# Kernel tuning notes

Measured on AMD Instinct MI355X. Metric: run time of the kernel, lower is better.

## Reference

```python
import jax, jax.numpy as jnp
import numpy as np

N_NODES = 18870
HIDDEN = 256
K = 20
HEAD_HIDDEN = 512
N_CLASSES = 3
N_GENES_OUT = 6640
B = 1024
FALLBACK_SCALE = 1e-3
LN_EPS = 1e-5


def setup_inputs() -> dict:
    key = jax.random.key(0)
    ks = jax.random.split(key, 8)
    node_idx = jax.random.randint(ks[0], (B,), 0, N_NODES)
    topk_neighbors = jax.random.randint(ks[1], (N_NODES, K), 0, N_NODES)
    node_emb = jax.random.normal(ks[2], (N_NODES, HIDDEN), dtype=jnp.float32)
    fallback_emb = jax.random.normal(ks[3], (HIDDEN,), dtype=jnp.float32) * 0.02
    w_attn = jax.random.normal(ks[4], (HIDDEN,), dtype=jnp.float32) * 0.02
    ln_gamma = jnp.ones((2 * HIDDEN,), dtype=jnp.float32)
    ln_beta = jnp.zeros((2 * HIDDEN,), dtype=jnp.float32)
    W1 = jax.random.normal(ks[5], (2 * HIDDEN, HEAD_HIDDEN), dtype=jnp.float32) * 0.02
    b1 = jnp.zeros((HEAD_HIDDEN,), dtype=jnp.float32)
    W2 = jax.random.normal(ks[6], (HEAD_HIDDEN, N_CLASSES * N_GENES_OUT), dtype=jnp.float32) * 0.02
    b2 = jnp.zeros((N_CLASSES * N_GENES_OUT,), dtype=jnp.float32)
    return dict(node_idx=node_idx, topk_neighbors=topk_neighbors, node_emb=node_emb,
                fallback_emb=fallback_emb, w_attn=w_attn, ln_gamma=ln_gamma, ln_beta=ln_beta,
                W1=W1, b1=b1, W2=W2, b2=b2)


def reference(node_idx, topk_neighbors, node_emb, fallback_emb, w_attn,
              ln_gamma, ln_beta, W1, b1, W2, b2):
    valid = node_idx >= 0                                   # [B]
    safe_idx = jnp.where(valid, node_idx, 0)                # [B]
    graph_emb = node_emb[safe_idx]                          # [B, H]
    pert_emb = jnp.where(valid[:, None],
                         graph_emb + FALLBACK_SCALE * fallback_emb[None, :],
                         fallback_emb[None, :])              # [B, H]

    nbr_idx = topk_neighbors[safe_idx]                      # [B, K]
    valid_nbr = nbr_idx >= 0                                # [B, K]
    nbr_emb = node_emb[jnp.clip(nbr_idx, 0)]                # [B, K, H]
    nbr_emb = nbr_emb * valid_nbr[..., None].astype(nbr_emb.dtype)

    # Faithful to the original broadcast: scores[b,k] = pert_emb[b,0] * (nbr_emb[b,k] . w_attn)
    scores = pert_emb[:, 0:1] * jnp.einsum('bkh,h->bk', nbr_emb, w_attn)  # [B, K]
    scores = jnp.where(valid_nbr, scores, -1e9)
    has_valid = jnp.any(valid_nbr, axis=1, keepdims=True)   # [B, 1]
    attn = jnp.where(has_valid, jax.nn.softmax(scores, axis=-1),
                     jnp.zeros_like(scores))                # [B, K]
    context = jnp.einsum('bk,bkh->bh', attn, nbr_emb)       # [B, H]

    combined = jnp.concatenate([pert_emb, context], axis=-1)  # [B, 2H]
    mu = jnp.mean(combined, axis=-1, keepdims=True)
    var = jnp.mean(jnp.square(combined - mu), axis=-1, keepdims=True)
    x = (combined - mu) * jax.lax.rsqrt(var + LN_EPS) * ln_gamma + ln_beta
    h = jax.nn.gelu(x @ W1 + b1, approximate=False)          # [B, HH]
    logits = h @ W2 + b2                                     # [B, 3*6640]
    return logits.reshape(-1, N_CLASSES, N_GENES_OUT)


if __name__ == '__main__':
    out = reference(**setup_inputs())
    print(out.shape)
```

## Files before the change

kernel.cpp:

```cpp
#include <hip/hip_runtime.h>
#include <hip/hip_bf16.h>
#include <math.h>

#define HIDDEN 256
#define K_NBR 20
#define NB 1024

typedef __bf16 bf16x8 __attribute__((ext_vector_type(8)));
typedef float f32x4 __attribute__((ext_vector_type(4)));

__device__ __forceinline__ float wave_sum(float v) {
#pragma unroll
    for (int o = 32; o > 0; o >>= 1) v += __shfl_xor(v, o, 64);
    return v;
}

__device__ __forceinline__ void gload16(const void* g, void* l) {
    __builtin_amdgcn_global_load_lds(
        (const __attribute__((address_space(1))) void*)g,
        (__attribute__((address_space(3))) void*)l, 16, 0, 0);
}

__device__ __forceinline__ int swz_chunk(int g, int row) {
    return (g & ~7) | ((g & 7) ^ (row & 7));
}

__device__ __forceinline__ void attn_ln_body(
    int b, int t, const int* __restrict__ node_idx, const int* __restrict__ topk,
    const float* __restrict__ node_emb, const float* __restrict__ fallback,
    const float* __restrict__ w_attn, const float* __restrict__ gamma,
    const float* __restrict__ beta, __bf16* __restrict__ xb, int swz_on,
    float* pe, float (*nbr)[HIDDEN], int* nidx, float* sc, float* red)
{
    int lane = t & 63, w = t >> 6;

    int nid = node_idx[b];
    bool valid = nid >= 0;
    int safe = valid ? nid : 0;

    pe[t] = valid ? node_emb[(size_t)safe * HIDDEN + t] + 1e-3f * fallback[t]
                  : fallback[t];
    if (t < K_NBR) nidx[t] = topk[safe * K_NBR + t];
    __syncthreads();

    for (int r = 0; r < K_NBR; ++r) {
        int gi = nidx[r];
        nbr[r][t] = (gi >= 0) ? node_emb[(size_t)gi * HIDDEN + t] : 0.f;
    }
    __syncthreads();

    float pe0 = pe[0];
    float wa[4];
#pragma unroll
    for (int q = 0; q < 4; ++q) wa[q] = w_attn[lane + 64 * q];
    for (int k = w; k < K_NBR; k += 4) {
        float p = 0.f;
#pragma unroll
        for (int q = 0; q < 4; ++q) p += nbr[k][lane + 64 * q] * wa[q];
        p = wave_sum(p);
        if (lane == 0) sc[k] = (nidx[k] >= 0) ? pe0 * p : -1e9f;
    }
    __syncthreads();

    bool has_valid = false;
#pragma unroll
    for (int k = 0; k < K_NBR; ++k) has_valid |= (nidx[k] >= 0);
    float mx = -1e30f;
#pragma unroll
    for (int k = 0; k < K_NBR; ++k) mx = fmaxf(mx, sc[k]);
    float at[K_NBR];
    float s = 0.f;
#pragma unroll
    for (int k = 0; k < K_NBR; ++k) { at[k] = expf(sc[k] - mx); s += at[k]; }
    float inv = has_valid ? 1.f / s : 0.f;

    float ctx = 0.f;
#pragma unroll
    for (int k = 0; k < K_NBR; ++k) ctx += (at[k] * inv) * nbr[k][t];

    float v0 = pe[t], v1 = ctx;
    float s1 = wave_sum(v0 + v1);
    float s2 = wave_sum(v0 * v0 + v1 * v1);
    if (lane == 0) { red[w] = s1; red[4 + w] = s2; }
    __syncthreads();
    s1 = red[0] + red[1] + red[2] + red[3];
    s2 = red[4] + red[5] + red[6] + red[7];
    float mu = s1 / 512.f;
    float var = s2 / 512.f - mu * mu;
    float rs = rsqrtf(var + 1e-5f);

    size_t base = (size_t)b * 512;
    int mask = swz_on ? (b & 7) : 0;
    {
        int e = t;
        int g = e >> 3, off = e & 7;
        int gp = (g & ~7) | ((g & 7) ^ mask);
        xb[base + gp * 8 + off] = (__bf16)((v0 - mu) * rs * gamma[t] + beta[t]);
        e = 256 + t;
        g = e >> 3;
        gp = (g & ~7) | ((g & 7) ^ mask);
        xb[base + gp * 8 + off] = (__bf16)((v1 - mu) * rs * gamma[256 + t] + beta[256 + t]);
    }
}

__device__ __forceinline__ void transpose_body(
    const float* __restrict__ Wm, __bf16* __restrict__ WT,
    int Kd, int Nd, int Np, int bx, int by, int t)
{
    int n = bx * 64 + (t >> 2);
    int k0 = by * 32 + (t & 3) * 8;
    bool ok = n < Nd;
    bf16x8 v;
#pragma unroll
    for (int j = 0; j < 8; ++j) {
        float f = ok ? Wm[(size_t)(k0 + j) * Nd + n] : 0.f;
        v[j] = (__bf16)f;
    }
    if (n < Np) {
        int gp = swz_chunk(k0 >> 3, n);
        *(bf16x8*)(WT + (size_t)n * Kd + gp * 8) = v;
    }
}

__global__ __launch_bounds__(256) void prep_kernel(
    const int* __restrict__ node_idx, const int* __restrict__ topk,
    const float* __restrict__ node_emb, const float* __restrict__ fallback,
    const float* __restrict__ w_attn, const float* __restrict__ gamma,
    const float* __restrict__ beta, const float* __restrict__ W1,
    const float* __restrict__ W2, __bf16* __restrict__ xb,
    __bf16* __restrict__ w1t, __bf16* __restrict__ w2t)
{
    __shared__ float pe[HIDDEN];
    __shared__ float nbr[K_NBR][HIDDEN];
    __shared__ int   nidx[K_NBR];
    __shared__ float sc[K_NBR];
    __shared__ float red[8];

    int bid = blockIdx.x;
    int t = threadIdx.x;
    if (bid < 4992) {
        transpose_body(W2, w2t, 512, 19920, 19968, bid % 312, bid / 312, t);
        return;
    }
    bid -= 4992;
    if (bid < 128) {
        transpose_body(W1, w1t, 512, 512, 512, bid % 8, bid / 8, t);
        return;
    }
    bid -= 128;
    attn_ln_body(bid, t, node_idx, topk, node_emb, fallback, w_attn, gamma, beta,
                 xb, 1, pe, nbr, nidx, sc, red);
}

__global__ __launch_bounds__(256) void attn_ln_kernel(
    const int* __restrict__ node_idx, const int* __restrict__ topk,
    const float* __restrict__ node_emb, const float* __restrict__ fallback,
    const float* __restrict__ w_attn, const float* __restrict__ gamma,
    const float* __restrict__ beta, __bf16* __restrict__ xb, int swz_on)
{
    __shared__ float pe[HIDDEN];
    __shared__ float nbr[K_NBR][HIDDEN];
    __shared__ int   nidx[K_NBR];
    __shared__ float sc[K_NBR];
    __shared__ float red[8];
    attn_ln_body(blockIdx.x, threadIdx.x, node_idx, topk, node_emb, fallback,
                 w_attn, gamma, beta, xb, swz_on, pe, nbr, nidx, sc, red);
}

__global__ __launch_bounds__(256, 4) void gemm1_kernel(
    const __bf16* __restrict__ A, const __bf16* __restrict__ BT,
    const float* __restrict__ bias, __bf16* __restrict__ Cb,
    int M, int N, int K)
{
    constexpr int BK = 64;
    __shared__ __bf16 As[2][64 * BK];
    __shared__ __bf16 Bs[2][64 * BK];

    int t = threadIdx.x;
    int lane = t & 63;
    int wid = t >> 6;
    int wm = wid >> 1, wn = wid & 1;
    int lo = lane & 15, hi = lane >> 4;

    int nwg = gridDim.x;
    int bid = blockIdx.x;
    int cpx = nwg >> 3;
    int lid = (bid & 7) * cpx + (bid >> 3);
    int m0 = (lid & 15) * 64;
    int n0 = (lid >> 4) * 64;

    int rsub = lane >> 3, kc = lane & 7;

    auto STAGE = [&](int buf, int k0) {
#pragma unroll
        for (int j = 0; j < 2; ++j) {
            int rb = j * 32 + wid * 8;
            gload16(A + (size_t)(m0 + rb + rsub) * K + k0 + kc * 8, &As[buf][rb * BK]);
        }
#pragma unroll
        for (int j = 0; j < 2; ++j) {
            int rb = j * 32 + wid * 8;
            gload16(BT + (size_t)(n0 + rb + rsub) * K + k0 + kc * 8, &Bs[buf][rb * BK]);
        }
    };

    f32x4 acc[2][2];
#pragma unroll
    for (int m = 0; m < 2; ++m)
#pragma unroll
        for (int n = 0; n < 2; ++n)
            acc[m][n] = (f32x4){0.f, 0.f, 0.f, 0.f};

    auto COMPUTE = [&](int buf) {
#pragma unroll
        for (int ks = 0; ks < 2; ++ks) {
            bf16x8 af[2], bfr[2];
#pragma unroll
            for (int m = 0; m < 2; ++m) {
                int r = wm * 32 + m * 16 + lo;
                af[m] = *(const bf16x8*)&As[buf][r * BK + (((ks * 4 + hi) ^ (r & 7)) * 8)];
            }
#pragma unroll
            for (int n = 0; n < 2; ++n) {
                int r = wn * 32 + n * 16 + lo;
                bfr[n] = *(const bf16x8*)&Bs[buf][r * BK + (((ks * 4 + hi) ^ (r & 7)) * 8)];
            }
#pragma unroll
            for (int m = 0; m < 2; ++m)
#pragma unroll
                for (int n = 0; n < 2; ++n)
                    acc[m][n] = __builtin_amdgcn_mfma_f32_16x16x32_bf16(
                        af[m], bfr[n], acc[m][n], 0, 0, 0);
        }
    };

    const int nt = K / BK;
    STAGE(0, 0);
    for (int tt = 0; tt < nt - 1; ++tt) {
        STAGE((tt + 1) & 1, (tt + 1) * BK);
        asm volatile("s_waitcnt vmcnt(4)" ::: "memory");
        __builtin_amdgcn_s_barrier();
        __builtin_amdgcn_sched_barrier(0);
        COMPUTE(tt & 1);
        __builtin_amdgcn_sched_barrier(0);
        __builtin_amdgcn_s_barrier();
    }
    asm volatile("s_waitcnt vmcnt(0)" ::: "memory");
    __builtin_amdgcn_s_barrier();
    __builtin_amdgcn_sched_barrier(0);
    COMPUTE((nt - 1) & 1);

#pragma unroll
    for (int m = 0; m < 2; ++m) {
        int gr = m0 + wm * 32 + m * 16 + hi * 4;
#pragma unroll
        for (int n = 0; n < 2; ++n) {
            int gc = n0 + wn * 32 + n * 16 + lo;
            float bv = bias[gc];
#pragma unroll
            for (int r = 0; r < 4; ++r) {
                float v = acc[m][n][r] + bv;
                float g = v * 0.5f * (1.f + erff(v * 0.70710678118f));
                int row = gr + r;
                int gp = swz_chunk(gc >> 3, row);
                Cb[(size_t)row * N + gp * 8 + (gc & 7)] = (__bf16)g;
            }
        }
    }
}

__global__ __launch_bounds__(512, 4) void gemm2_kernel(
    const __bf16* __restrict__ A, const __bf16* __restrict__ BT,
    const float* __restrict__ bias, float* __restrict__ C,
    int M, int N, int K)
{
    constexpr int BK = 64;
    __shared__ __bf16 As[2][128 * BK];
    __shared__ __bf16 Bs[2][128 * BK];

    int t = threadIdx.x;
    int lane = t & 63;
    int wid = t >> 6;
    int wm = wid >> 2, wn = wid & 3;
    int lo = lane & 15, hi = lane >> 4;

    int nwg = gridDim.x;
    int bid = blockIdx.x;
    int cpx = nwg >> 3;
    int lid = (bid & 7) * cpx + (bid >> 3);
    int m0 = (lid & 7) * 128;
    int n0 = (lid >> 3) * 128;

    int rsub = lane >> 3, kc = lane & 7;

    auto STAGE = [&](int buf, int k0) {
#pragma unroll
        for (int j = 0; j < 2; ++j) {
            int rb = j * 64 + wid * 8;
            gload16(A + (size_t)(m0 + rb + rsub) * K + k0 + kc * 8, &As[buf][rb * BK]);
        }
#pragma unroll
        for (int j = 0; j < 2; ++j) {
            int rb = j * 64 + wid * 8;
            gload16(BT + (size_t)(n0 + rb + rsub) * K + k0 + kc * 8, &Bs[buf][rb * BK]);
        }
    };

    f32x4 acc[4][2];
#pragma unroll
    for (int m = 0; m < 4; ++m)
#pragma unroll
        for (int n = 0; n < 2; ++n)
            acc[m][n] = (f32x4){0.f, 0.f, 0.f, 0.f};

    auto COMPUTE = [&](int buf) {
#pragma unroll
        for (int ks = 0; ks < 2; ++ks) {
            bf16x8 af[4], bfr[2];
#pragma unroll
            for (int m = 0; m < 4; ++m) {
                int r = wm * 64 + m * 16 + lo;
                af[m] = *(const bf16x8*)&As[buf][r * BK + (((ks * 4 + hi) ^ (r & 7)) * 8)];
            }
#pragma unroll
            for (int n = 0; n < 2; ++n) {
                int r = wn * 32 + n * 16 + lo;
                bfr[n] = *(const bf16x8*)&Bs[buf][r * BK + (((ks * 4 + hi) ^ (r & 7)) * 8)];
            }
#pragma unroll
            for (int m = 0; m < 4; ++m)
#pragma unroll
                for (int n = 0; n < 2; ++n)
                    acc[m][n] = __builtin_amdgcn_mfma_f32_16x16x32_bf16(
                        af[m], bfr[n], acc[m][n], 0, 0, 0);
        }
    };

    const int nt = K / BK;
    STAGE(0, 0);
    for (int tt = 0; tt < nt - 1; ++tt) {
        STAGE((tt + 1) & 1, (tt + 1) * BK);
        asm volatile("s_waitcnt vmcnt(4)" ::: "memory");
        __builtin_amdgcn_s_barrier();
        __builtin_amdgcn_sched_barrier(0);
        COMPUTE(tt & 1);
        __builtin_amdgcn_sched_barrier(0);
        __builtin_amdgcn_s_barrier();
    }
    asm volatile("s_waitcnt vmcnt(0)" ::: "memory");
    __builtin_amdgcn_s_barrier();
    __builtin_amdgcn_sched_barrier(0);
    COMPUTE((nt - 1) & 1);

#pragma unroll
    for (int m = 0; m < 4; ++m) {
        int gr = m0 + wm * 64 + m * 16 + hi * 4;
#pragma unroll
        for (int n = 0; n < 2; ++n) {
            int gc = n0 + wn * 32 + n * 16 + lo;
            if (gc < N) {
                float bv = bias[gc];
#pragma unroll
                for (int r = 0; r < 4; ++r)
                    C[(size_t)(gr + r) * N + gc] = acc[m][n][r] + bv;
            }
        }
    }
}

template<bool GELU>
__global__ __launch_bounds__(256) void gemm_kernel(
    const __bf16* __restrict__ A, const float* __restrict__ Bm,
    const float* __restrict__ bias, float* __restrict__ Cf, __bf16* __restrict__ Cb,
    int M, int N, int K)
{
    constexpr int BK = 64;
    __shared__ bf16x8 As[2][128 * 8];
    __shared__ bf16x8 Bs[2][128 * 8];

    int t = threadIdx.x;
    int lane = t & 63;
    int wid = t >> 6;
    int wm = wid >> 1, wn = wid & 1;
    int lo = lane & 15, hi = lane >> 4;

    int n0 = blockIdx.x * 128;
    int m0 = blockIdx.y * 128;

    int cA = t & 7;
    int rA = t >> 3;
    int nl = t & 127;
    int kcb = t >> 7;

    bf16x8 a_st[4];
    bf16x8 b_st[4];

    auto LOAD = [&](int k0) {
#pragma unroll
        for (int i = 0; i < 4; ++i)
            a_st[i] = *(const bf16x8*)(A + (size_t)(m0 + rA + 32 * i) * K + k0 + cA * 8);
        int col = n0 + nl;
        bool ok = col < N;
#pragma unroll
        for (int i = 0; i < 4; ++i) {
            int kcv = kcb + 2 * i;
            bf16x8 v;
#pragma unroll
            for (int j = 0; j < 8; ++j) {
                float f = ok ? Bm[(size_t)(k0 + kcv * 8 + j) * N + col] : 0.f;
                v[j] = (__bf16)f;
            }
            b_st[i] = v;
        }
    };
    auto WRITE = [&](int buf) {
#pragma unroll
        for (int i = 0; i < 4; ++i) {
            int r = rA + 32 * i;
            As[buf][r * 8 + (cA ^ (r & 7))] = a_st[i];
        }
#pragma unroll
        for (int i = 0; i < 4; ++i) {
            int kcv = kcb + 2 * i;
            Bs[buf][nl * 8 + (kcv ^ (nl & 7))] = b_st[i];
        }
    };

    f32x4 acc[4][4];
#pragma unroll
    for (int m = 0; m < 4; ++m)
#pragma unroll
        for (int n = 0; n < 4; ++n)
            acc[m][n] = (f32x4){0.f, 0.f, 0.f, 0.f};

    auto COMPUTE = [&](int buf) {
#pragma unroll
        for (int ks = 0; ks < 2; ++ks) {
            bf16x8 af[4], bfr[4];
#pragma unroll
            for (int m = 0; m < 4; ++m) {
                int r = wm * 64 + m * 16 + lo;
                af[m] = As[buf][r * 8 + ((ks * 4 + hi) ^ (r & 7))];
            }
#pragma unroll
            for (int n = 0; n < 4; ++n) {
                int r = wn * 64 + n * 16 + lo;
                bfr[n] = Bs[buf][r * 8 + ((ks * 4 + hi) ^ (r & 7))];
            }
#pragma unroll
            for (int m = 0; m < 4; ++m)
#pragma unroll
                for (int n = 0; n < 4; ++n)
                    acc[m][n] = __builtin_amdgcn_mfma_f32_16x16x32_bf16(
                        af[m], bfr[n], acc[m][n], 0, 0, 0);
        }
    };

    const int nt = K / BK;
    LOAD(0);
    WRITE(0);
    __syncthreads();
    for (int tt = 0; tt < nt; ++tt) {
        int cur = tt & 1;
        if (tt + 1 < nt) LOAD((tt + 1) * BK);
        COMPUTE(cur);
        if (tt + 1 < nt) WRITE(cur ^ 1);
        __syncthreads();
    }

#pragma unroll
    for (int m = 0; m < 4; ++m) {
        int gr = m0 + wm * 64 + m * 16 + hi * 4;
#pragma unroll
        for (int n = 0; n < 4; ++n) {
            int gc = n0 + wn * 64 + n * 16 + lo;
            if (gc < N) {
                float bv = bias[gc];
#pragma unroll
                for (int r = 0; r < 4; ++r) {
                    float v = acc[m][n][r] + bv;
                    if constexpr (GELU) {
                        float g = v * 0.5f * (1.f + erff(v * 0.70710678118f));
                        Cb[(size_t)(gr + r) * N + gc] = (__bf16)g;
                    } else {
                        Cf[(size_t)(gr + r) * N + gc] = v;
                    }
                }
            }
        }
    }
}

extern "C" void kernel_launch(void* const* d_in, const int* in_sizes, int n_in,
                              void* d_out, int out_size, void* d_ws, size_t ws_size,
                              hipStream_t stream) {
    const int*   node_idx = (const int*)d_in[0];
    const int*   topk     = (const int*)d_in[1];
    const float* node_emb = (const float*)d_in[2];
    const float* fallback = (const float*)d_in[3];
    const float* w_attn   = (const float*)d_in[4];
    const float* gamma    = (const float*)d_in[5];
    const float* beta     = (const float*)d_in[6];
    const float* W1       = (const float*)d_in[7];
    const float* b1       = (const float*)d_in[8];
    const float* W2       = (const float*)d_in[9];
    const float* b2       = (const float*)d_in[10];
    float* out = (float*)d_out;

    const int M = 1024, Kd = 512, N1 = 512, N2 = 19920;
    const int N2p = 19968;

    __bf16* xb  = (__bf16*)d_ws;
    __bf16* h   = xb + (size_t)M * Kd;
    __bf16* w1t = h + (size_t)M * Kd;
    __bf16* w2t = w1t + (size_t)N1 * Kd;
    size_t needed = ((size_t)2 * M * Kd + (size_t)N1 * Kd + (size_t)N2p * Kd) * sizeof(__bf16);

    if (ws_size >= needed) {
        prep_kernel<<<4992 + 128 + 1024, 256, 0, stream>>>(
            node_idx, topk, node_emb, fallback, w_attn, gamma, beta, W1, W2,
            xb, w1t, w2t);

        gemm1_kernel<<<dim3(128), 256, 0, stream>>>(
            xb, w1t, b1, h, M, N1, Kd);

        gemm2_kernel<<<dim3(1248), 512, 0, stream>>>(
            h, w2t, b2, out, M, N2, Kd);
    } else {
        attn_ln_kernel<<<NB, 256, 0, stream>>>(node_idx, topk, node_emb, fallback,
                                               w_attn, gamma, beta, xb, 0);
        gemm_kernel<true><<<dim3(4, 8), 256, 0, stream>>>(
            xb, W1, b1, nullptr, h, M, N1, Kd);
        gemm_kernel<false><<<dim3(156, 8), 256, 0, stream>>>(
            h, W2, b2, out, nullptr, M, N2, Kd);
    }
}
```

Measured before the change: 74.73 us.

## Fuse prep, GEMM1 and GEMM2 into one persistent cooperative kernel with grid syncs

Replaces the three launches (prep/transpose, gemm1, gemm2) with one persistent cooperative kernel of 512-thread blocks. It loops over work units and separates the stages with grid-wide syncs. Attention is processed two rows per block, the W2 transpose uses nontemporal loads, and GEMM1 tiles widen to 64x128. The goal is to remove launch overhead and the tail bubbles between kernels, at the cost of grid-sync latency and limited occupancy from the 64 KB shared memory. It falls back to the old three-kernel path if the cooperative launch fails.

```diff
diff --git a/kernel.cpp b/kernel.cpp
--- a/kernel.cpp
+++ b/kernel.cpp
@@ -1,6 +1,9 @@
 #include <hip/hip_runtime.h>
 #include <hip/hip_bf16.h>
+#include <hip/hip_cooperative_groups.h>
 #include <math.h>
+
+namespace cg = cooperative_groups;
 
 #define HIDDEN 256
 #define K_NBR 20
@@ -21,8 +24,335 @@
         (__attribute__((address_space(3))) void*)l, 16, 0, 0);
 }
 
-__device__ __forceinline__ int swz_chunk(int g, int row) {
+__device__ __forceinline__ int swz3(int g, int row) {
     return (g & ~7) | ((g & 7) ^ (row & 7));
+}
+
+struct AttnSmem {
+    float pe[2][HIDDEN];
+    float nbr[2][K_NBR][HIDDEN];
+    int   nidx[2][K_NBR];
+    float sc[2][K_NBR];
+    float red[2][8];
+};
+
+__device__ void attn2_unit(int p, int t,
+    const int* node_idx, const int* topk, const float* node_emb,
+    const float* fallback, const float* w_attn, const float* gamma,
+    const float* beta, __bf16* xb, void* smem)
+{
+    AttnSmem& S = *(AttnSmem*)smem;
+    int s = t >> 8, tl = t & 255;
+    int lane = tl & 63, w = tl >> 6;
+    int b = p * 2 + s;
+
+    int nid = node_idx[b];
+    bool valid = nid >= 0;
+    int safe = valid ? nid : 0;
+
+    S.pe[s][tl] = valid ? node_emb[(size_t)safe * HIDDEN + tl] + 1e-3f * fallback[tl]
+                        : fallback[tl];
+    if (tl < K_NBR) S.nidx[s][tl] = topk[safe * K_NBR + tl];
+    __syncthreads();
+
+    for (int r = 0; r < K_NBR; ++r) {
+        int gi = S.nidx[s][r];
+        S.nbr[s][r][tl] = (gi >= 0) ? node_emb[(size_t)gi * HIDDEN + tl] : 0.f;
+    }
+    __syncthreads();
+
+    float pe0 = S.pe[s][0];
+    float wa[4];
+#pragma unroll
+    for (int q = 0; q < 4; ++q) wa[q] = w_attn[lane + 64 * q];
+    for (int k = w; k < K_NBR; k += 4) {
+        float pp = 0.f;
+#pragma unroll
+        for (int q = 0; q < 4; ++q) pp += S.nbr[s][k][lane + 64 * q] * wa[q];
+        pp = wave_sum(pp);
+        if (lane == 0) S.sc[s][k] = (S.nidx[s][k] >= 0) ? pe0 * pp : -1e9f;
+    }
+    __syncthreads();
+
+    bool has_valid = false;
+#pragma unroll
+    for (int k = 0; k < K_NBR; ++k) has_valid |= (S.nidx[s][k] >= 0);
+    float mx = -1e30f;
+#pragma unroll
+    for (int k = 0; k < K_NBR; ++k) mx = fmaxf(mx, S.sc[s][k]);
+    float at[K_NBR];
+    float sm = 0.f;
+#pragma unroll
+    for (int k = 0; k < K_NBR; ++k) { at[k] = expf(S.sc[s][k] - mx); sm += at[k]; }
+    float inv = has_valid ? 1.f / sm : 0.f;
+
+    float ctx = 0.f;
+#pragma unroll
+    for (int k = 0; k < K_NBR; ++k) ctx += (at[k] * inv) * S.nbr[s][k][tl];
+
+    float v0 = S.pe[s][tl], v1 = ctx;
+    float s1 = wave_sum(v0 + v1);
+    float s2 = wave_sum(v0 * v0 + v1 * v1);
+    if (lane == 0) { S.red[s][w] = s1; S.red[s][4 + w] = s2; }
+    __syncthreads();
+    s1 = S.red[s][0] + S.red[s][1] + S.red[s][2] + S.red[s][3];
+    s2 = S.red[s][4] + S.red[s][5] + S.red[s][6] + S.red[s][7];
+    float mu = s1 / 512.f;
+    float var = s2 / 512.f - mu * mu;
+    float rs = rsqrtf(var + 1e-5f);
+
+    size_t base = (size_t)b * 512;
+    int mask = b & 7;
+    {
+        int e = tl;
+        int g = e >> 3, off = e & 7;
+        int gp = (g & ~7) | ((g & 7) ^ mask);
+        xb[base + gp * 8 + off] = (__bf16)((v0 - mu) * rs * gamma[tl] + beta[tl]);
+        e = 256 + tl;
+        g = e >> 3;
+        gp = (g & ~7) | ((g & 7) ^ mask);
+        xb[base + gp * 8 + off] = (__bf16)((v1 - mu) * rs * gamma[256 + tl] + beta[256 + tl]);
+    }
+    __syncthreads();
+}
+
+__device__ void transpose_unit(const float* __restrict__ Wm, __bf16* __restrict__ WT,
+                               int Kd, int Nd, int Np, int ux, int uy, int t)
+{
+    int n = ux * 128 + (t >> 2);
+    int k0 = uy * 32 + (t & 3) * 8;
+    bool ok = n < Nd;
+    bf16x8 v;
+#pragma unroll
+    for (int j = 0; j < 8; ++j) {
+        float f = ok ? __builtin_nontemporal_load(&Wm[(size_t)(k0 + j) * Nd + n]) : 0.f;
+        v[j] = (__bf16)f;
+    }
+    if (n < Np) {
+        int gp = swz3(k0 >> 3, n);
+        *(bf16x8*)(WT + (size_t)n * Kd + gp * 8) = v;
+    }
+}
+
+__device__ void gemm1_tile(int bid, int t, void* smem,
+    const __bf16* __restrict__ A, const __bf16* __restrict__ BT,
+    const float* __restrict__ bias, __bf16* __restrict__ Cb)
+{
+    const int K = 512, N = 512;
+    __bf16* As = (__bf16*)smem;
+    __bf16* Bs = (__bf16*)smem + 8192;
+
+    int lane = t & 63, wid = t >> 6;
+    int wm = wid >> 2, wn = wid & 3;
+    int lo = lane & 15, hi = lane >> 4;
+    int m0 = (bid & 15) * 64;
+    int n0 = (bid >> 4) * 128;
+    int rsub = lane >> 3, kc = lane & 7;
+
+    auto STAGE = [&](int buf, int k0) {
+        gload16(A + (size_t)(m0 + wid * 8 + rsub) * K + k0 + kc * 8,
+                &As[buf * 4096 + wid * 512]);
+#pragma unroll
+        for (int j = 0; j < 2; ++j) {
+            int rb = j * 64 + wid * 8;
+            gload16(BT + (size_t)(n0 + rb + rsub) * K + k0 + kc * 8,
+                    &Bs[buf * 8192 + rb * 64]);
+        }
+    };
+
+    f32x4 acc[2][2];
+#pragma unroll
+    for (int m = 0; m < 2; ++m)
+#pragma unroll
+        for (int n = 0; n < 2; ++n)
+            acc[m][n] = (f32x4){0.f, 0.f, 0.f, 0.f};
+
+    auto COMPUTE = [&](int buf) {
+#pragma unroll
+        for (int ks = 0; ks < 2; ++ks) {
+            bf16x8 af[2], bfr[2];
+#pragma unroll
+            for (int m = 0; m < 2; ++m) {
+                int r = wm * 32 + m * 16 + lo;
+                af[m] = *(const bf16x8*)&As[buf * 4096 + r * 64 + (((ks * 4 + hi) ^ (r & 7)) * 8)];
+            }
+#pragma unroll
+            for (int n = 0; n < 2; ++n) {
+                int r = wn * 32 + n * 16 + lo;
+                bfr[n] = *(const bf16x8*)&Bs[buf * 8192 + r * 64 + (((ks * 4 + hi) ^ (r & 7)) * 8)];
+            }
+#pragma unroll
+            for (int m = 0; m < 2; ++m)
+#pragma unroll
+                for (int n = 0; n < 2; ++n)
+                    acc[m][n] = __builtin_amdgcn_mfma_f32_16x16x32_bf16(
+                        af[m], bfr[n], acc[m][n], 0, 0, 0);
+        }
+    };
+
+    const int nt = K / 64;
+    STAGE(0, 0);
+    for (int tt = 0; tt < nt - 1; ++tt) {
+        STAGE((tt + 1) & 1, (tt + 1) * 64);
+        asm volatile("s_waitcnt vmcnt(3)" ::: "memory");
+        __builtin_amdgcn_s_barrier();
+        __builtin_amdgcn_sched_barrier(0);
+        COMPUTE(tt & 1);
+        __builtin_amdgcn_sched_barrier(0);
+        __builtin_amdgcn_s_barrier();
+    }
+    asm volatile("s_waitcnt vmcnt(0)" ::: "memory");
+    __builtin_amdgcn_s_barrier();
+    __builtin_amdgcn_sched_barrier(0);
+    COMPUTE((nt - 1) & 1);
+    __builtin_amdgcn_s_barrier();
+
+#pragma unroll
+    for (int m = 0; m < 2; ++m) {
+        int gr = m0 + wm * 32 + m * 16 + hi * 4;
+#pragma unroll
+        for (int n = 0; n < 2; ++n) {
+            int gc = n0 + wn * 32 + n * 16 + lo;
+            float bv = bias[gc];
+#pragma unroll
+            for (int r = 0; r < 4; ++r) {
+                float v = acc[m][n][r] + bv;
+                float g = v * 0.5f * (1.f + erff(v * 0.70710678118f));
+                int row = gr + r;
+                int gp = swz3(gc >> 3, row);
+                Cb[(size_t)row * N + gp * 8 + (gc & 7)] = (__bf16)g;
+            }
+        }
+    }
+}
+
+__device__ void gemm2_tile(int tile, int t, void* smem,
+    const __bf16* __restrict__ A, const __bf16* __restrict__ BT,
+    const float* __restrict__ bias, float* __restrict__ C, int N)
+{
+    const int K = 512;
+    __bf16* As = (__bf16*)smem;
+    __bf16* Bs = (__bf16*)smem + 16384;
+
+    int lane = t & 63, wid = t >> 6;
+    int wm = wid >> 2, wn = wid & 3;
+    int lo = lane & 15, hi = lane >> 4;
+
+    int lid = (tile & 7) * 156 + (tile >> 3);
+    int m0 = (lid & 7) * 128;
+    int n0 = (lid >> 3) * 128;
+
+    int rsub = lane >> 3, kc = lane & 7;
+
+    auto STAGE = [&](int buf, int k0) {
+#pragma unroll
+        for (int j = 0; j < 2; ++j) {
+            int rb = j * 64 + wid * 8;
+            gload16(A + (size_t)(m0 + rb + rsub) * K + k0 + kc * 8, &As[buf * 8192 + rb * 64]);
+        }
+#pragma unroll
+        for (int j = 0; j < 2; ++j) {
+            int rb = j * 64 + wid * 8;
+            gload16(BT + (size_t)(n0 + rb + rsub) * K + k0 + kc * 8, &Bs[buf * 8192 + rb * 64]);
+        }
+    };
+
+    f32x4 acc[4][2];
+#pragma unroll
+    for (int m = 0; m < 4; ++m)
+#pragma unroll
+        for (int n = 0; n < 2; ++n)
+            acc[m][n] = (f32x4){0.f, 0.f, 0.f, 0.f};
+
+    auto COMPUTE = [&](int buf) {
+#pragma unroll
+        for (int ks = 0; ks < 2; ++ks) {
+            bf16x8 af[4], bfr[2];
+#pragma unroll
+            for (int m = 0; m < 4; ++m) {
+                int r = wm * 64 + m * 16 + lo;
+                af[m] = *(const bf16x8*)&As[buf * 8192 + r * 64 + (((ks * 4 + hi) ^ (r & 7)) * 8)];
+            }
+#pragma unroll
+            for (int n = 0; n < 2; ++n) {
+                int r = wn * 32 + n * 16 + lo;
+                bfr[n] = *(const bf16x8*)&Bs[buf * 8192 + r * 64 + (((ks * 4 + hi) ^ (r & 7)) * 8)];
+            }
+#pragma unroll
+            for (int m = 0; m < 4; ++m)
+#pragma unroll
+                for (int n = 0; n < 2; ++n)
+                    acc[m][n] = __builtin_amdgcn_mfma_f32_16x16x32_bf16(
+                        af[m], bfr[n], acc[m][n], 0, 0, 0);
+        }
+    };
+
+    const int nt = K / 64;
+    STAGE(0, 0);
+    for (int tt = 0; tt < nt - 1; ++tt) {
+        STAGE((tt + 1) & 1, (tt + 1) * 64);
+        asm volatile("s_waitcnt vmcnt(4)" ::: "memory");
+        __builtin_amdgcn_s_barrier();
+        __builtin_amdgcn_sched_barrier(0);
+        COMPUTE(tt & 1);
+        __builtin_amdgcn_sched_barrier(0);
+        __builtin_amdgcn_s_barrier();
+    }
+    asm volatile("s_waitcnt vmcnt(0)" ::: "memory");
+    __builtin_amdgcn_s_barrier();
+    __builtin_amdgcn_sched_barrier(0);
+    COMPUTE((nt - 1) & 1);
+    __builtin_amdgcn_s_barrier();
+
+#pragma unroll
+    for (int m = 0; m < 4; ++m) {
+        int gr = m0 + wm * 64 + m * 16 + hi * 4;
+#pragma unroll
+        for (int n = 0; n < 2; ++n) {
+            int gc = n0 + wn * 32 + n * 16 + lo;
+            if (gc < N) {
+                float bv = bias[gc];
+#pragma unroll
+                for (int r = 0; r < 4; ++r)
+                    C[(size_t)(gr + r) * N + gc] = acc[m][n][r] + bv;
+            }
+        }
+    }
+}
+
+__global__ __launch_bounds__(512, 4) void fused_kernel(
+    const int* node_idx, const int* topk, const float* node_emb,
+    const float* fallback, const float* w_attn, const float* gamma,
+    const float* beta, const float* W1, const float* b1,
+    const float* W2, const float* b2,
+    __bf16* xb, __bf16* w1t, __bf16* w2t, __bf16* h, float* out)
+{
+    __shared__ __align__(16) unsigned char SMEM[65536];
+    int t = threadIdx.x;
+    int bid = blockIdx.x;
+    int nblk = gridDim.x;
+
+    for (int u = bid; u < 3072; u += nblk) {
+        if (u < 2496) {
+            transpose_unit(W2, w2t, 512, 19920, 19968, u % 156, u / 156, t);
+        } else if (u < 3008) {
+            attn2_unit(u - 2496, t, node_idx, topk, node_emb, fallback,
+                       w_attn, gamma, beta, xb, SMEM);
+        } else {
+            int v = u - 3008;
+            transpose_unit(W1, w1t, 512, 512, 512, v & 3, v >> 2, t);
+        }
+    }
+    __threadfence();
+    cg::this_grid().sync();
+
+    for (int g1 = bid; g1 < 64; g1 += nblk)
+        gemm1_tile(g1, t, SMEM, xb, w1t, b1, h);
+    __threadfence();
+    cg::this_grid().sync();
+
+    for (int tile = bid; tile < 1248; tile += nblk)
+        gemm2_tile(tile, t, SMEM, h, w2t, b2, out, 19920);
 }
 
 __device__ __forceinline__ void attn_ln_body(
@@ -33,7 +363,6 @@
     float* pe, float (*nbr)[HIDDEN], int* nidx, float* sc, float* red)
 {
     int lane = t & 63, w = t >> 6;
-
     int nid = node_idx[b];
     bool valid = nid >= 0;
     int safe = valid ? nid : 0;
@@ -42,13 +371,11 @@
                   : fallback[t];
     if (t < K_NBR) nidx[t] = topk[safe * K_NBR + t];
     __syncthreads();
-
     for (int r = 0; r < K_NBR; ++r) {
         int gi = nidx[r];
         nbr[r][t] = (gi >= 0) ? node_emb[(size_t)gi * HIDDEN + t] : 0.f;
     }
     __syncthreads();
-
     float pe0 = pe[0];
     float wa[4];
 #pragma unroll
@@ -61,7 +388,6 @@
         if (lane == 0) sc[k] = (nidx[k] >= 0) ? pe0 * p : -1e9f;
     }
     __syncthreads();
-
     bool has_valid = false;
 #pragma unroll
     for (int k = 0; k < K_NBR; ++k) has_valid |= (nidx[k] >= 0);
@@ -73,11 +399,9 @@
 #pragma unroll
     for (int k = 0; k < K_NBR; ++k) { at[k] = expf(sc[k] - mx); s += at[k]; }
     float inv = has_valid ? 1.f / s : 0.f;
-
     float ctx = 0.f;
 #pragma unroll
     for (int k = 0; k < K_NBR; ++k) ctx += (at[k] * inv) * nbr[k][t];
-
     float v0 = pe[t], v1 = ctx;
     float s1 = wave_sum(v0 + v1);
     float s2 = wave_sum(v0 * v0 + v1 * v1);
@@ -88,7 +412,6 @@
     float mu = s1 / 512.f;
     float var = s2 / 512.f - mu * mu;
     float rs = rsqrtf(var + 1e-5f);
-
     size_t base = (size_t)b * 512;
     int mask = swz_on ? (b & 7) : 0;
     {
@@ -117,7 +440,7 @@
         v[j] = (__bf16)f;
     }
     if (n < Np) {
-        int gp = swz_chunk(k0 >> 3, n);
+        int gp = swz3(k0 >> 3, n);
         *(bf16x8*)(WT + (size_t)n * Kd + gp * 8) = v;
     }
 }
@@ -135,36 +458,14 @@
     __shared__ int   nidx[K_NBR];
     __shared__ float sc[K_NBR];
     __shared__ float red[8];
-
     int bid = blockIdx.x;
     int t = threadIdx.x;
-    if (bid < 4992) {
-        transpose_body(W2, w2t, 512, 19920, 19968, bid % 312, bid / 312, t);
-        return;
-    }
+    if (bid < 4992) { transpose_body(W2, w2t, 512, 19920, 19968, bid % 312, bid / 312, t); return; }
     bid -= 4992;
-    if (bid < 128) {
-        transpose_body(W1, w1t, 512, 512, 512, bid % 8, bid / 8, t);
-        return;
-    }
+    if (bid < 128) { transpose_body(W1, w1t, 512, 512, 512, bid % 8, bid / 8, t); return; }
     bid -= 128;
     attn_ln_body(bid, t, node_idx, topk, node_emb, fallback, w_attn, gamma, beta,
                  xb, 1, pe, nbr, nidx, sc, red);
-}
-
-__global__ __launch_bounds__(256) void attn_ln_kernel(
-    const int* __restrict__ node_idx, const int* __restrict__ topk,
-    const float* __restrict__ node_emb, const float* __restrict__ fallback,
-    const float* __restrict__ w_attn, const float* __restrict__ gamma,
-    const float* __restrict__ beta, __bf16* __restrict__ xb, int swz_on)
-{
-    __shared__ float pe[HIDDEN];
-    __shared__ float nbr[K_NBR][HIDDEN];
-    __shared__ int   nidx[K_NBR];
-    __shared__ float sc[K_NBR];
-    __shared__ float red[8];
-    attn_ln_body(blockIdx.x, threadIdx.x, node_idx, topk, node_emb, fallback,
-                 w_attn, gamma, beta, xb, swz_on, pe, nbr, nidx, sc, red);
 }
 
 __global__ __launch_bounds__(256, 4) void gemm1_kernel(
@@ -175,22 +476,16 @@
     constexpr int BK = 64;
     __shared__ __bf16 As[2][64 * BK];
     __shared__ __bf16 Bs[2][64 * BK];
-
     int t = threadIdx.x;
-    int lane = t & 63;
-    int wid = t >> 6;
+    int lane = t & 63, wid = t >> 6;
     int wm = wid >> 1, wn = wid & 1;
     int lo = lane & 15, hi = lane >> 4;
-
-    int nwg = gridDim.x;
-    int bid = blockIdx.x;
+    int nwg = gridDim.x, bid = blockIdx.x;
     int cpx = nwg >> 3;
     int lid = (bid & 7) * cpx + (bid >> 3);
     int m0 = (lid & 15) * 64;
     int n0 = (lid >> 4) * 64;
-
     int rsub = lane >> 3, kc = lane & 7;
-
     auto STAGE = [&](int buf, int k0) {
 #pragma unroll
         for (int j = 0; j < 2; ++j) {
@@ -203,14 +498,11 @@
             gload16(BT + (size_t)(n0 + rb + rsub) * K + k0 + kc * 8, &Bs[buf][rb * BK]);
         }
     };
-
     f32x4 acc[2][2];
 #pragma unroll
     for (int m = 0; m < 2; ++m)
 #pragma unroll
-        for (int n = 0; n < 2; ++n)
-            acc[m][n] = (f32x4){0.f, 0.f, 0.f, 0.f};
-
+        for (int n = 0; n < 2; ++n) acc[m][n] = (f32x4){0.f, 0.f, 0.f, 0.f};
     auto COMPUTE = [&](int buf) {
 #pragma unroll
         for (int ks = 0; ks < 2; ++ks) {
@@ -233,7 +525,6 @@
                         af[m], bfr[n], acc[m][n], 0, 0, 0);
         }
     };
-
     const int nt = K / BK;
     STAGE(0, 0);
     for (int tt = 0; tt < nt - 1; ++tt) {
@@ -249,7 +540,6 @@
     __builtin_amdgcn_s_barrier();
     __builtin_amdgcn_sched_barrier(0);
     COMPUTE((nt - 1) & 1);
-
 #pragma unroll
     for (int m = 0; m < 2; ++m) {
         int gr = m0 + wm * 32 + m * 16 + hi * 4;
@@ -262,7 +552,7 @@
                 float v = acc[m][n][r] + bv;
                 float g = v * 0.5f * (1.f + erff(v * 0.70710678118f));
                 int row = gr + r;
-                int gp = swz_chunk(gc >> 3, row);
+                int gp = swz3(gc >> 3, row);
                 Cb[(size_t)row * N + gp * 8 + (gc & 7)] = (__bf16)g;
             }
         }
@@ -274,221 +564,11 @@
     const float* __restrict__ bias, float* __restrict__ C,
     int M, int N, int K)
 {
-    constexpr int BK = 64;
-    __shared__ __bf16 As[2][128 * BK];
-    __shared__ __bf16 Bs[2][128 * BK];
-
+    __shared__ __align__(16) unsigned char SMEM[65536];
     int t = threadIdx.x;
-    int lane = t & 63;
-    int wid = t >> 6;
-    int wm = wid >> 2, wn = wid & 3;
-    int lo = lane & 15, hi = lane >> 4;
-
-    int nwg = gridDim.x;
-    int bid = blockIdx.x;
-    int cpx = nwg >> 3;
-    int lid = (bid & 7) * cpx + (bid >> 3);
-    int m0 = (lid & 7) * 128;
-    int n0 = (lid >> 3) * 128;
-
-    int rsub = lane >> 3, kc = lane & 7;
-
-    auto STAGE = [&](int buf, int k0) {
-#pragma unroll
-        for (int j = 0; j < 2; ++j) {
-            int rb = j * 64 + wid * 8;
-            gload16(A + (size_t)(m0 + rb + rsub) * K + k0 + kc * 8, &As[buf][rb * BK]);
-        }
-#pragma unroll
-        for (int j = 0; j < 2; ++j) {
-            int rb = j * 64 + wid * 8;
-            gload16(BT + (size_t)(n0 + rb + rsub) * K + k0 + kc * 8, &Bs[buf][rb * BK]);
-        }
-    };
-
-    f32x4 acc[4][2];
-#pragma unroll
-    for (int m = 0; m < 4; ++m)
-#pragma unroll
-        for (int n = 0; n < 2; ++n)
-            acc[m][n] = (f32x4){0.f, 0.f, 0.f, 0.f};
-
-    auto COMPUTE = [&](int buf) {
-#pragma unroll
-        for (int ks = 0; ks < 2; ++ks) {
-            bf16x8 af[4], bfr[2];
-#pragma unroll
-            for (int m = 0; m < 4; ++m) {
-                int r = wm * 64 + m * 16 + lo;
-                af[m] = *(const bf16x8*)&As[buf][r * BK + (((ks * 4 + hi) ^ (r & 7)) * 8)];
-            }
-#pragma unroll
-            for (int n = 0; n < 2; ++n) {
-                int r = wn * 32 + n * 16 + lo;
-                bfr[n] = *(const bf16x8*)&Bs[buf][r * BK + (((ks * 4 + hi) ^ (r & 7)) * 8)];
-            }
-#pragma unroll
-            for (int m = 0; m < 4; ++m)
-#pragma unroll
-                for (int n = 0; n < 2; ++n)
-                    acc[m][n] = __builtin_amdgcn_mfma_f32_16x16x32_bf16(
-                        af[m], bfr[n], acc[m][n], 0, 0, 0);
-        }
-    };
-
-    const int nt = K / BK;
-    STAGE(0, 0);
-    for (int tt = 0; tt < nt - 1; ++tt) {
-        STAGE((tt + 1) & 1, (tt + 1) * BK);
-        asm volatile("s_waitcnt vmcnt(4)" ::: "memory");
-        __builtin_amdgcn_s_barrier();
-        __builtin_amdgcn_sched_barrier(0);
-        COMPUTE(tt & 1);
-        __builtin_amdgcn_sched_barrier(0);
-        __builtin_amdgcn_s_barrier();
-    }
-    asm volatile("s_waitcnt vmcnt(0)" ::: "memory");
-    __builtin_amdgcn_s_barrier();
-    __builtin_amdgcn_sched_barrier(0);
-    COMPUTE((nt - 1) & 1);
-
-#pragma unroll
-    for (int m = 0; m < 4; ++m) {
-        int gr = m0 + wm * 64 + m * 16 + hi * 4;
-#pragma unroll
-        for (int n = 0; n < 2; ++n) {
-            int gc = n0 + wn * 32 + n * 16 + lo;
-            if (gc < N) {
-                float bv = bias[gc];
-#pragma unroll
-                for (int r = 0; r < 4; ++r)
-                    C[(size_t)(gr + r) * N + gc] = acc[m][n][r] + bv;
-            }
-        }
-    }
-}
-
-template<bool GELU>
-__global__ __launch_bounds__(256) void gemm_kernel(
-    const __bf16* __restrict__ A, const float* __restrict__ Bm,
-    const float* __restrict__ bias, float* __restrict__ Cf, __bf16* __restrict__ Cb,
-    int M, int N, int K)
-{
-    constexpr int BK = 64;
-    __shared__ bf16x8 As[2][128 * 8];
-    __shared__ bf16x8 Bs[2][128 * 8];
-
-    int t = threadIdx.x;
-    int lane = t & 63;
-    int wid = t >> 6;
-    int wm = wid >> 1, wn = wid & 1;
-    int lo = lane & 15, hi = lane >> 4;
-
-    int n0 = blockIdx.x * 128;
-    int m0 = blockIdx.y * 128;
-
-    int cA = t & 7;
-    int rA = t >> 3;
-    int nl = t & 127;
-    int kcb = t >> 7;
-
-    bf16x8 a_st[4];
-    bf16x8 b_st[4];
-
-    auto LOAD = [&](int k0) {
-#pragma unroll
-        for (int i = 0; i < 4; ++i)
-            a_st[i] = *(const bf16x8*)(A + (size_t)(m0 + rA + 32 * i) * K + k0 + cA * 8);
-        int col = n0 + nl;
-        bool ok = col < N;
-#pragma unroll
-        for (int i = 0; i < 4; ++i) {
-            int kcv = kcb + 2 * i;
-            bf16x8 v;
-#pragma unroll
-            for (int j = 0; j < 8; ++j) {
-                float f = ok ? Bm[(size_t)(k0 + kcv * 8 + j) * N + col] : 0.f;
-                v[j] = (__bf16)f;
-            }
-            b_st[i] = v;
-        }
-    };
-    auto WRITE = [&](int buf) {
-#pragma unroll
-        for (int i = 0; i < 4; ++i) {
-            int r = rA + 32 * i;
-            As[buf][r * 8 + (cA ^ (r & 7))] = a_st[i];
-        }
-#pragma unroll
-        for (int i = 0; i < 4; ++i) {
-            int kcv = kcb + 2 * i;
-            Bs[buf][nl * 8 + (kcv ^ (nl & 7))] = b_st[i];
-        }
-    };
-
-    f32x4 acc[4][4];
-#pragma unroll
-    for (int m = 0; m < 4; ++m)
-#pragma unroll
-        for (int n = 0; n < 4; ++n)
-            acc[m][n] = (f32x4){0.f, 0.f, 0.f, 0.f};
-
-    auto COMPUTE = [&](int buf) {
-#pragma unroll
-        for (int ks = 0; ks < 2; ++ks) {
-            bf16x8 af[4], bfr[4];
-#pragma unroll
-            for (int m = 0; m < 4; ++m) {
-                int r = wm * 64 + m * 16 + lo;
-                af[m] = As[buf][r * 8 + ((ks * 4 + hi) ^ (r & 7))];
-            }
-#pragma unroll
-            for (int n = 0; n < 4; ++n) {
-                int r = wn * 64 + n * 16 + lo;
-                bfr[n] = Bs[buf][r * 8 + ((ks * 4 + hi) ^ (r & 7))];
-            }
-#pragma unroll
-            for (int m = 0; m < 4; ++m)
-#pragma unroll
-                for (int n = 0; n < 4; ++n)
-                    acc[m][n] = __builtin_amdgcn_mfma_f32_16x16x32_bf16(
-                        af[m], bfr[n], acc[m][n], 0, 0, 0);
-        }
-    };
-
-    const int nt = K / BK;
-    LOAD(0);
-    WRITE(0);
-    __syncthreads();
-    for (int tt = 0; tt < nt; ++tt) {
-        int cur = tt & 1;
-        if (tt + 1 < nt) LOAD((tt + 1) * BK);
-        COMPUTE(cur);
-        if (tt + 1 < nt) WRITE(cur ^ 1);
-        __syncthreads();
-    }
-
-#pragma unroll
-    for (int m = 0; m < 4; ++m) {
-        int gr = m0 + wm * 64 + m * 16 + hi * 4;
-#pragma unroll
-        for (int n = 0; n < 4; ++n) {
-            int gc = n0 + wn * 64 + n * 16 + lo;
-            if (gc < N) {
-                float bv = bias[gc];
-#pragma unroll
-                for (int r = 0; r < 4; ++r) {
-                    float v = acc[m][n][r] + bv;
-                    if constexpr (GELU) {
-                        float g = v * 0.5f * (1.f + erff(v * 0.70710678118f));
-                        Cb[(size_t)(gr + r) * N + gc] = (__bf16)g;
-                    } else {
-                        Cf[(size_t)(gr + r) * N + gc] = v;
-                    }
-                }
-            }
-        }
-    }
+    int nwg = gridDim.x, bid = blockIdx.x;
+    gemm2_tile(bid, t, SMEM, A, BT, bias, C, N);
+    (void)nwg; (void)M; (void)K;
 }
 
 extern "C" void kernel_launch(void* const* d_in, const int* in_sizes, int n_in,
@@ -517,21 +597,38 @@
     size_t needed = ((size_t)2 * M * Kd + (size_t)N1 * Kd + (size_t)N2p * Kd) * sizeof(__bf16);
 
     if (ws_size >= needed) {
+        int occ = 0;
+        hipError_t e0 = hipOccupancyMaxActiveBlocksPerMultiprocessor(
+            &occ, fused_kernel, 512, 0);
+        int grid = (e0 == hipSuccess && occ > 0) ? (occ * 256 < 512 ? occ * 256 : 512) : 0;
+        bool coop_ok = false;
+        if (grid >= 64) {
+            void* args[] = { (void*)&node_idx, (void*)&topk, (void*)&node_emb,
+                             (void*)&fallback, (void*)&w_attn, (void*)&gamma,
+                             (void*)&beta, (void*)&W1, (void*)&b1,
+                             (void*)&W2, (void*)&b2,
+                             (void*)&xb, (void*)&w1t, (void*)&w2t, (void*)&h,
+                             (void*)&out };
+            hipError_t e = hipLaunchCooperativeKernel(
+                (const void*)fused_kernel, dim3(grid), dim3(512), args, 0, stream);
+            coop_ok = (e == hipSuccess);
+        }
+        if (!coop_ok) {
+            prep_kernel<<<4992 + 128 + 1024, 256, 0, stream>>>(
+                node_idx, topk, node_emb, fallback, w_attn, gamma, beta, W1, W2,
+                xb, w1t, w2t);
+            gemm1_kernel<<<dim3(128), 256, 0, stream>>>(
+                xb, w1t, b1, h, M, N1, Kd);
+            gemm2_kernel<<<dim3(1248), 512, 0, stream>>>(
+                h, w2t, b2, out, M, N2, Kd);
+        }
+    } else {
         prep_kernel<<<4992 + 128 + 1024, 256, 0, stream>>>(
             node_idx, topk, node_emb, fallback, w_attn, gamma, beta, W1, W2,
             xb, w1t, w2t);
-
         gemm1_kernel<<<dim3(128), 256, 0, stream>>>(
             xb, w1t, b1, h, M, N1, Kd);
-
         gemm2_kernel<<<dim3(1248), 512, 0, stream>>>(
             h, w2t, b2, out, M, N2, Kd);
-    } else {
-        attn_ln_kernel<<<NB, 256, 0, stream>>>(node_idx, topk, node_emb, fallback,
-                                               w_attn, gamma, beta, xb, 0);
-        gemm_kernel<true><<<dim3(4, 8), 256, 0, stream>>>(
-            xb, W1, b1, nullptr, h, M, N1, Kd);
-        gemm_kernel<false><<<dim3(156, 8), 256, 0, stream>>>(
-            h, W2, b2, out, nullptr, M, N2, Kd);
-    }
-}
+    }
+}
```

Result: slower. 265.5 us (+255.3%).
